# Performance work log

Measured on AMD Instinct MI355X. Metric: run time of the kernel, lower is better.

The kernel has to match this reference:

```python
import jax, jax.numpy as jnp
import numpy as np

N_NODES = 50000
N_EDGES = 640000
D = 128
BN_EPS = 1e-5


def setup_inputs() -> dict:
    key = jax.random.key(0)
    k1, k2, k3 = jax.random.split(key, 3)
    x = jax.random.normal(k1, (N_NODES, D), dtype=jnp.float32)
    # Glorot-ish weight for GCNConv linear
    W = jax.random.normal(k2, (D, D), dtype=jnp.float32) * (1.0 / np.sqrt(D))
    b = jnp.zeros((D,), dtype=jnp.float32)
    gamma = jnp.ones((D,), dtype=jnp.float32)
    beta = jnp.zeros((D,), dtype=jnp.float32)
    edge_index = jax.random.randint(k3, (2, N_EDGES), 0, N_NODES, dtype=jnp.int64)
    return {"x": x, "W": W, "b": b, "gamma": gamma, "beta": beta, "edge_index": edge_index}


def reference(x, W, b, gamma, beta, edge_index):
    N = x.shape[0]
    # --- GCNConv: x' = D^{-1/2} (A + I) D^{-1/2} (x W) + b ---
    xw = x @ W  # [N, D]
    loops = jnp.arange(N, dtype=edge_index.dtype)
    src = jnp.concatenate([edge_index[0], loops])  # [E+N]
    dst = jnp.concatenate([edge_index[1], loops])
    ones = jnp.ones(src.shape[0], dtype=x.dtype)
    deg = jax.ops.segment_sum(ones, dst, num_segments=N)  # in-degree incl. self-loop
    dinv = jnp.where(deg > 0, jax.lax.rsqrt(deg), 0.0)
    norm = dinv[src] * dinv[dst]  # [E+N]
    msg = xw[src] * norm[:, None]  # [E+N, D] gathered + scaled messages
    h = jax.ops.segment_sum(msg, dst, num_segments=N) + b  # scatter-add aggregation
    # --- BatchNorm1d (training-mode batch stats over nodes, biased var) ---
    mean = jnp.mean(h, axis=0)
    var = jnp.mean(jnp.square(h - mean), axis=0)
    h = (h - mean) * jax.lax.rsqrt(var + BN_EPS) * gamma + beta
    # --- activation (relu) ---
    h = jax.nn.relu(h)
    # --- residual (in_channels == out_channels) ---
    h = x + h
    # --- dropout: identity in eval mode for deterministic reference ---
    return h
```

## Files before the change

kernel.cpp:

```cpp
#include <hip/hip_runtime.h>

#define DCH 128
#define ROWS 16
#define BN_EPS 1e-5f

typedef unsigned short u16;
typedef __attribute__((ext_vector_type(8))) short short8;
typedef __attribute__((ext_vector_type(4))) float floatx4;

__device__ __forceinline__ float bf2f(u16 u) {
    return __uint_as_float(((unsigned)u) << 16);
}
__device__ __forceinline__ u16 f2bf(float f) {
    unsigned u = __float_as_uint(f);
    u += 0x7FFFu + ((u >> 16) & 1u);
    return (u16)(u >> 16);
}
__device__ __forceinline__ float ldf(const void* p, int i, int isbf) {
    return isbf ? bf2f(((const u16*)p)[i]) : ((const float*)p)[i];
}

__global__ void prep_kernel(const int* ei, int ewords, const u16* xw, int* ws_i,
                            const void* W, u16* Wb, float* zbase, int zn) {
    int t = threadIdx.x;
    if (blockIdx.x == 0) {
        __shared__ int s_nz, s_hits;
        if (t == 0) { s_nz = 0; s_hits = 0; }
        __syncthreads();
        int nz = 0;
        for (int i = t; i < 1024; i += 256) {
            int w = 2 * i + 1;
            if (w < ewords) nz |= ei[w];
        }
        if (nz) atomicOr(&s_nz, 1);
        unsigned m = (xw[2 * t] >> 8) & 0x7F;
        if (m >= 0x3B && m <= 0x43) atomicAdd(&s_hits, 1);
        __syncthreads();
        int isbf = (s_hits >= 128) ? 1 : 0;
        if (t == 0) {
            ws_i[0] = (s_nz == 0) ? 1 : 0;
            ws_i[1] = isbf;
            ws_i[2] = 0;
        }
        for (int idx = t; idx < DCH * DCH; idx += 256) {
            int j = idx & 7, lane = (idx >> 3) & 63, kk = (idx >> 9) & 3, nt = idx >> 11;
            int k = kk * 32 + (lane >> 4) * 8 + j;
            int n = nt * 16 + (lane & 15);
            Wb[idx] = f2bf(ldf(W, k * DCH + n, isbf));
        }
    } else {
        int stride = (gridDim.x - 1) * 256;
        for (int i = (blockIdx.x - 1) * 256 + t; i < zn; i += stride) zbase[i] = 0.f;
    }
}

__global__ void zero_kernel(float* p, int n) {
    int stride = gridDim.x * 256;
    for (int i = blockIdx.x * 256 + threadIdx.x; i < n; i += stride) p[i] = 0.f;
}

__global__ void paint_kernel(u16* out, int n, unsigned val) {
    int stride = gridDim.x * 256;
    for (int i = blockIdx.x * 256 + threadIdx.x; i < n; i += stride) out[i] = (u16)val;
}

__global__ void detect_kernel(const int* ei, int ewords, const u16* xw, int* ws_i) {
    __shared__ int s_nz, s_hits;
    int t = threadIdx.x;
    if (t == 0) { s_nz = 0; s_hits = 0; }
    __syncthreads();
    int nz = 0;
    for (int i = t; i < 1024; i += 256) {
        int w = 2 * i + 1;
        if (w < ewords) nz |= ei[w];
    }
    if (nz) atomicOr(&s_nz, 1);
    unsigned m = (xw[2 * t] >> 8) & 0x7F;
    if (m >= 0x3B && m <= 0x43) atomicAdd(&s_hits, 1);
    __syncthreads();
    if (t == 0) {
        ws_i[0] = (s_nz == 0) ? 1 : 0;
        ws_i[1] = (s_hits >= 128) ? 1 : 0;
        ws_i[2] = 0;
    }
}

__global__ void deg_kernel(const int* ei, int E, int* ws_i, int* deg, int N) {
    int is64 = ws_i[0];
    int i = blockIdx.x * 256 + threadIdx.x;
    int e0 = 2 * i;
    if (e0 >= E) return;
    int d0, d1 = -1, s0, s1 = 0;
    if (is64) {
        int4 sp = *(const int4*)&ei[2 * e0];
        int4 dp = *(const int4*)&ei[2 * E + 2 * e0];
        s0 = sp.x; s1 = sp.z; d0 = dp.x; d1 = dp.z;
    } else {
        int2 sp = *(const int2*)&ei[e0];
        int2 dp = *(const int2*)&ei[E + e0];
        s0 = sp.x; s1 = sp.y; d0 = dp.x; d1 = dp.y;
    }
    if (((unsigned)s0 >= (unsigned)N) || ((unsigned)d0 >= (unsigned)N))
        atomicOr(&ws_i[2], 2);
    atomicAdd(&deg[min(max(d0, 0), N - 1)], 1);
    if (e0 + 1 < E) {
        if (((unsigned)s1 >= (unsigned)N) || ((unsigned)d1 >= (unsigned)N))
            atomicOr(&ws_i[2], 2);
        atomicAdd(&deg[min(max(d1, 0), N - 1)], 1);
    }
}

__global__ void dinv_kernel(const int* deg, float* dinv, int N, int* ws_i) {
    int i = blockIdx.x * 256 + threadIdx.x;
    if (i < N) {
        float v = rsqrtf((float)(deg[i] + 1));
        if (!(v > 0.f && v <= 1.001f)) atomicOr(&ws_i[2], 4);
        dinv[i] = v;
    }
}

__global__ void scanA_kernel(const int* deg, int* part, int N) {
    int base = blockIdx.x * 1024 + threadIdx.x * 4;
    int s = 0;
    #pragma unroll
    for (int j = 0; j < 4; ++j) {
        int i = base + j;
        if (i < N) s += deg[i];
    }
    #pragma unroll
    for (int o = 1; o < 64; o <<= 1) s += __shfl_xor(s, o, 64);
    __shared__ int ws4[4];
    if ((threadIdx.x & 63) == 0) ws4[threadIdx.x >> 6] = s;
    __syncthreads();
    if (threadIdx.x == 0) part[blockIdx.x] = ws4[0] + ws4[1] + ws4[2] + ws4[3];
}

__global__ void scanB_kernel(int* part, int P) {
    __shared__ int wsum[4];
    int t = threadIdx.x, lane = t & 63, w = t >> 6;
    int v = (t < P) ? part[t] : 0;
    int sc = v;
    #pragma unroll
    for (int o = 1; o < 64; o <<= 1) {
        int u = __shfl_up(sc, o, 64);
        if (lane >= o) sc += u;
    }
    if (lane == 63) wsum[w] = sc;
    __syncthreads();
    if (t < 4) {
        int s = wsum[t];
        #pragma unroll
        for (int o = 1; o < 4; o <<= 1) {
            int u = __shfl_up(s, o, 4);
            if (t >= o) s += u;
        }
        wsum[t] = s;
    }
    __syncthreads();
    int excl = sc - v + (w ? wsum[w - 1] : 0);
    if (t < P) part[t] = excl;
}

__global__ void scanC_kernel(int* deg_cursor, const int* part, int* rowptr,
                             float* dinv, int N) {
    __shared__ int wsum[4];
    int t = threadIdx.x, lane = t & 63, w = t >> 6;
    int base = blockIdx.x * 1024 + t * 4;
    int v[4], ts = 0;
    #pragma unroll
    for (int j = 0; j < 4; ++j) {
        int i = base + j;
        v[j] = (i < N) ? deg_cursor[i] : 0;
        ts += v[j];
    }
    int sc = ts;
    #pragma unroll
    for (int o = 1; o < 64; o <<= 1) {
        int u = __shfl_up(sc, o, 64);
        if (lane >= o) sc += u;
    }
    if (lane == 63) wsum[w] = sc;
    __syncthreads();
    if (t < 4) {
        int s = wsum[t];
        #pragma unroll
        for (int o = 1; o < 4; o <<= 1) {
            int u = __shfl_up(s, o, 4);
            if (t >= o) s += u;
        }
        wsum[t] = s;
    }
    __syncthreads();
    int run = sc - ts + (w ? wsum[w - 1] : 0) + part[blockIdx.x];
    #pragma unroll
    for (int j = 0; j < 4; ++j) {
        int i = base + j;
        if (i < N) {
            deg_cursor[i] = run;
            run += v[j];
            rowptr[i + 1] = run;
            dinv[i] = rsqrtf((float)(v[j] + 1));
        }
    }
    if (blockIdx.x == 0 && t == 0) rowptr[0] = 0;
}

__global__ void fillcsr_kernel(const int* ei, int E, const int* ws_i,
                               int* cursor, int* col, int N) {
    int is64 = ws_i[0];
    int i = blockIdx.x * 256 + threadIdx.x;
    int e0 = 2 * i;
    if (e0 >= E) return;
    int d0, d1 = 0, s0, s1 = 0;
    if (is64) {
        int4 sp = *(const int4*)&ei[2 * e0];
        int4 dp = *(const int4*)&ei[2 * E + 2 * e0];
        s0 = sp.x; s1 = sp.z; d0 = dp.x; d1 = dp.z;
    } else {
        int2 sp = *(const int2*)&ei[e0];
        int2 dp = *(const int2*)&ei[E + e0];
        s0 = sp.x; s1 = sp.y; d0 = dp.x; d1 = dp.y;
    }
    s0 = min(max(s0, 0), N - 1);
    d0 = min(max(d0, 0), N - 1);
    int pos0 = atomicAdd(&cursor[d0], 1);
    col[pos0] = s0;
    if (e0 + 1 < E) {
        s1 = min(max(s1, 0), N - 1);
        d1 = min(max(d1, 0), N - 1);
        int pos1 = atomicAdd(&cursor[d1], 1);
        col[pos1] = s1;
    }
}

__global__ void gemm_mfma_kernel(const void* x, const u16* Wb, const float* dinv,
                                 const int* ws_i, u16* y, int N) {
    int isbf = ws_i[1];
    int t = threadIdx.x;
    int wv = t >> 6, lane = t & 63;
    int quad = lane >> 4, l16 = lane & 15;
    int r0 = blockIdx.x * 64 + wv * 16;
    int rl = min(r0 + l16, N - 1);
    short8 a[4];
    if (isbf) {
        const u16* xp = (const u16*)x + (size_t)rl * DCH + quad * 8;
        #pragma unroll
        for (int kk = 0; kk < 4; ++kk)
            a[kk] = *(const short8*)(xp + kk * 32);
    } else {
        const float* xp = (const float*)x + (size_t)rl * DCH + quad * 8;
        #pragma unroll
        for (int kk = 0; kk < 4; ++kk) {
            float4 f0 = *(const float4*)(xp + kk * 32);
            float4 f1 = *(const float4*)(xp + kk * 32 + 4);
            short8 aa;
            aa[0] = (short)f2bf(f0.x); aa[1] = (short)f2bf(f0.y);
            aa[2] = (short)f2bf(f0.z); aa[3] = (short)f2bf(f0.w);
            aa[4] = (short)f2bf(f1.x); aa[5] = (short)f2bf(f1.y);
            aa[6] = (short)f2bf(f1.z); aa[7] = (short)f2bf(f1.w);
            a[kk] = aa;
        }
    }
    floatx4 acc[8];
    #pragma unroll
    for (int i = 0; i < 8; ++i) acc[i] = (floatx4)(0.f);
    #pragma unroll
    for (int nt = 0; nt < 8; ++nt) {
        #pragma unroll
        for (int kk = 0; kk < 4; ++kk) {
            short8 bfr = *(const short8*)&Wb[(((nt << 2) | kk) * 64 + lane) * 8];
            acc[nt] = __builtin_amdgcn_mfma_f32_16x16x32_bf16(a[kk], bfr, acc[nt], 0, 0, 0);
        }
    }
    #pragma unroll
    for (int i = 0; i < 4; ++i) {
        int row = r0 + quad * 4 + i;
        if (row < N) {
            float dv = dinv[row];
            #pragma unroll
            for (int nt = 0; nt < 8; ++nt)
                y[(size_t)row * DCH + nt * 16 + l16] = f2bf(acc[nt][i] * dv);
        }
    }
}

__global__ __launch_bounds__(256, 8)
void gather_stats_kernel(const int* rowptr, const int* col, const u16* y,
                         const float* dinv, const void* b, const int* ws_i,
                         float* h, float* sums, float* sumsq, int N) {
    int isbf = ws_i[1];
    int t = threadIdx.x;
    int hw = t >> 5;
    int l32 = t & 31;
    int c0 = l32 * 4;
    float bb[4];
    #pragma unroll
    for (int k = 0; k < 4; ++k) bb[k] = ldf(b, c0 + k, isbf);
    float ps[4] = {0.f, 0.f, 0.f, 0.f}, pq[4] = {0.f, 0.f, 0.f, 0.f};
    int stream_id = blockIdx.x * 8 + hw;
    int nstreams = gridDim.x * 8;
    for (int n = stream_id; n < N; n += nstreams) {
        uint2 qs = *(const uint2*)&y[(size_t)n * DCH + c0];
        float a0[4] = { bf2f((u16)(qs.x & 0xFFFF)), bf2f((u16)(qs.x >> 16)),
                        bf2f((u16)(qs.y & 0xFFFF)), bf2f((u16)(qs.y >> 16)) };
        float a1[4] = {0.f, 0.f, 0.f, 0.f};
        float a2[4] = {0.f, 0.f, 0.f, 0.f};
        float a3[4] = {0.f, 0.f, 0.f, 0.f};
        int beg = rowptr[n], end = rowptr[n + 1];
        int j = beg;
        for (; j + 3 < end; j += 4) {
            int s0 = col[j], s1 = col[j + 1], s2 = col[j + 2], s3 = col[j + 3];
            uint2 q0 = *(const uint2*)&y[(size_t)s0 * DCH + c0];
            uint2 q1 = *(const uint2*)&y[(size_t)s1 * DCH + c0];
            uint2 q2 = *(const uint2*)&y[(size_t)s2 * DCH + c0];
            uint2 q3 = *(const uint2*)&y[(size_t)s3 * DCH + c0];
            a0[0] += bf2f((u16)(q0.x & 0xFFFF)); a0[1] += bf2f((u16)(q0.x >> 16));
            a0[2] += bf2f((u16)(q0.y & 0xFFFF)); a0[3] += bf2f((u16)(q0.y >> 16));
            a1[0] += bf2f((u16)(q1.x & 0xFFFF)); a1[1] += bf2f((u16)(q1.x >> 16));
            a1[2] += bf2f((u16)(q1.y & 0xFFFF)); a1[3] += bf2f((u16)(q1.y >> 16));
            a2[0] += bf2f((u16)(q2.x & 0xFFFF)); a2[1] += bf2f((u16)(q2.x >> 16));
            a2[2] += bf2f((u16)(q2.y & 0xFFFF)); a2[3] += bf2f((u16)(q2.y >> 16));
            a3[0] += bf2f((u16)(q3.x & 0xFFFF)); a3[1] += bf2f((u16)(q3.x >> 16));
            a3[2] += bf2f((u16)(q3.y & 0xFFFF)); a3[3] += bf2f((u16)(q3.y >> 16));
        }
        for (; j < end; ++j) {
            uint2 q0 = *(const uint2*)&y[(size_t)col[j] * DCH + c0];
            a0[0] += bf2f((u16)(q0.x & 0xFFFF)); a0[1] += bf2f((u16)(q0.x >> 16));
            a0[2] += bf2f((u16)(q0.y & 0xFFFF)); a0[3] += bf2f((u16)(q0.y >> 16));
        }
        float dn = dinv[n];
        float4 o;
        o.x = fmaf((a0[0] + a1[0]) + (a2[0] + a3[0]), dn, bb[0]);
        o.y = fmaf((a0[1] + a1[1]) + (a2[1] + a3[1]), dn, bb[1]);
        o.z = fmaf((a0[2] + a1[2]) + (a2[2] + a3[2]), dn, bb[2]);
        o.w = fmaf((a0[3] + a1[3]) + (a2[3] + a3[3]), dn, bb[3]);
        *(float4*)&h[(size_t)n * DCH + c0] = o;
        ps[0] += o.x; pq[0] += o.x * o.x;
        ps[1] += o.y; pq[1] += o.y * o.y;
        ps[2] += o.z; pq[2] += o.z * o.z;
        ps[3] += o.w; pq[3] += o.w * o.w;
    }
    __shared__ float lps[8][DCH], lpq[8][DCH];
    #pragma unroll
    for (int k = 0; k < 4; ++k) { lps[hw][c0 + k] = ps[k]; lpq[hw][c0 + k] = pq[k]; }
    __syncthreads();
    if (t < DCH) {
        int ch = (t + blockIdx.x * 16) & 127;
        float s = 0.f, q = 0.f;
        #pragma unroll
        for (int i = 0; i < 8; ++i) { s += lps[i][ch]; q += lpq[i][ch]; }
        atomicAdd(&sums[ch], s);
        atomicAdd(&sumsq[ch], q);
    }
}

__global__ void gemm_valu_kernel(const void* x, const void* W, const float* dinv,
                                 const int* ws_i, void* y, int N) {
    __shared__ float WsF[64 * DCH];
    __shared__ float xs[ROWS * DCH];
    int isbf = ws_i[1];
    int t = threadIdx.x;
    int r0 = blockIdx.x * ROWS;
    for (int i = t; i < ROWS * DCH; i += 256) {
        int r = r0 + (i >> 7);
        xs[i] = (r < N) ? ldf(x, r * DCH + (i & 127), isbf) : 0.f;
    }
    int d = t & 127, rh = t >> 7;
    float s[8];
    #pragma unroll
    for (int j = 0; j < 8; ++j) s[j] = 0.f;
    for (int half = 0; half < 2; ++half) {
        __syncthreads();
        for (int i = t; i < 64 * DCH; i += 256)
            WsF[i] = ldf(W, half * 64 * DCH + i, isbf);
        __syncthreads();
        #pragma unroll
        for (int j = 0; j < 8; ++j) {
            int rr = rh + 2 * j;
            float a = s[j];
            #pragma unroll 16
            for (int k = 0; k < 64; ++k)
                a = fmaf(xs[rr * DCH + half * 64 + k], WsF[k * DCH + d], a);
            s[j] = a;
        }
    }
    #pragma unroll
    for (int j = 0; j < 8; ++j) {
        int r = r0 + rh + 2 * j;
        if (r < N) {
            float v = s[j] * dinv[r];
            if (isbf) ((u16*)y)[r * DCH + d] = f2bf(v);
            else      ((float*)y)[r * DCH + d] = v;
        }
    }
}

__global__ void scatter_kernel(const int* ei, int E, const int* ws_i,
                               const void* y, float* acc, int N) {
    int is64 = ws_i[0], isbf = ws_i[1];
    int gid = blockIdx.x * 256 + threadIdx.x;
    int e = gid >> 5;
    if (e >= E) return;
    int c0 = (gid & 31) * 4;
    int s = is64 ? ei[2 * e] : ei[e];
    int d = is64 ? ei[2 * E + 2 * e] : ei[E + e];
    s = min(max(s, 0), N - 1);
    d = min(max(d, 0), N - 1);
    float v0, v1, v2, v3;
    if (isbf) {
        uint2 raw = *(const uint2*)&((const u16*)y)[s * DCH + c0];
        v0 = bf2f((u16)(raw.x & 0xFFFF)); v1 = bf2f((u16)(raw.x >> 16));
        v2 = bf2f((u16)(raw.y & 0xFFFF)); v3 = bf2f((u16)(raw.y >> 16));
    } else {
        float4 raw = *(const float4*)&((const float*)y)[s * DCH + c0];
        v0 = raw.x; v1 = raw.y; v2 = raw.z; v3 = raw.w;
    }
    float* a = &acc[d * DCH + c0];
    atomicAdd(a + 0, v0);
    atomicAdd(a + 1, v1);
    atomicAdd(a + 2, v2);
    atomicAdd(a + 3, v3);
}

__global__ void bnstat_kernel(const void* y, float* acc, const float* dinv,
                              const void* b, int* ws_i,
                              float* sums, float* sumsq, int total) {
    int isbf = ws_i[1];
    int t = threadIdx.x;
    int d = t & 127;
    float bb = ldf(b, d, isbf);
    float ps = 0.f, pq = 0.f;
    int stride = gridDim.x * 256;
    for (int i = blockIdx.x * 256 + t; i < total; i += stride) {
        int r = i >> 7;
        float yv = isbf ? bf2f(((const u16*)y)[i]) : ((const float*)y)[i];
        float v = (yv + acc[i]) * dinv[r] + bb;
        acc[i] = v;
        ps += v;
        pq += v * v;
    }
    __shared__ float ls[256], lq[256];
    ls[t] = ps; lq[t] = pq;
    __syncthreads();
    if (t < 128) {
        atomicAdd(&sums[d], ls[t] + ls[t + 128]);
        atomicAdd(&sumsq[d], lq[t] + lq[t + 128]);
    }
}

__global__ void out_kernel(const float* h, const void* x,
                           const void* gamma, const void* beta,
                           int* ws_i, const float* sums, const float* sumsq,
                           void* out, int total, float invN) {
    __shared__ float sc[DCH], sh[DCH];
    int isbf = ws_i[1];
    int t = threadIdx.x;
    if (t < DCH) {
        float mean = sums[t] * invN;
        float var = fmaxf(sumsq[t] * invN - mean * mean, 0.f);
        float s = ldf(gamma, t, isbf) * rsqrtf(var + BN_EPS);
        if (!(var < 1e8f && fabsf(s) < 1e6f)) atomicOr(&ws_i[2], 32);
        sc[t] = s;
        sh[t] = ldf(beta, t, isbf) - mean * s;
    }
    __syncthreads();
    int total4 = total >> 2;
    int stride = gridDim.x * 256;
    for (int i4 = blockIdx.x * 256 + t; i4 < total4; i4 += stride) {
        int i = i4 * 4;
        int d = i & 127;
        float4 hv = *(const float4*)&h[i];
        float v0 = fmaf(hv.x, sc[d], sh[d]);
        float v1 = fmaf(hv.y, sc[d + 1], sh[d + 1]);
        float v2 = fmaf(hv.z, sc[d + 2], sh[d + 2]);
        float v3 = fmaf(hv.w, sc[d + 3], sh[d + 3]);
        if (isbf) {
            uint2 xv = *(const uint2*)&((const u16*)x)[i];
            v0 = fmaxf(v0, 0.f) + bf2f((u16)(xv.x & 0xFFFF));
            v1 = fmaxf(v1, 0.f) + bf2f((u16)(xv.x >> 16));
            v2 = fmaxf(v2, 0.f) + bf2f((u16)(xv.y & 0xFFFF));
            v3 = fmaxf(v3, 0.f) + bf2f((u16)(xv.y >> 16));
            uint2 ov;
            ov.x = (unsigned)f2bf(v0) | ((unsigned)f2bf(v1) << 16);
            ov.y = (unsigned)f2bf(v2) | ((unsigned)f2bf(v3) << 16);
            *(uint2*)&((u16*)out)[i] = ov;
        } else {
            float4 xv = *(const float4*)&((const float*)x)[i];
            float4 ov;
            ov.x = fmaxf(v0, 0.f) + xv.x;
            ov.y = fmaxf(v1, 0.f) + xv.y;
            ov.z = fmaxf(v2, 0.f) + xv.z;
            ov.w = fmaxf(v3, 0.f) + xv.w;
            *(float4*)&((float*)out)[i] = ov;
        }
    }
}

__global__ void diag_kernel(const int* ws_i, void* out, int n) {
    int e = ws_i[2];
    if (!e) return;
    int isbf = ws_i[1];
    float v = 4096.f + 32.f * (float)(e & 63);
    int stride = gridDim.x * 256;
    if (isbf) {
        u16 code = f2bf(v);
        for (int i = blockIdx.x * 256 + threadIdx.x; i < n; i += stride)
            ((u16*)out)[i] = code;
    } else {
        for (int i = blockIdx.x * 256 + threadIdx.x; i < n; i += stride)
            ((float*)out)[i] = v;
    }
}

extern "C" void kernel_launch(void* const* d_in, const int* in_sizes, int n_in,
                              void* d_out, int out_size, void* d_ws, size_t ws_size,
                              hipStream_t stream) {
    const void* x     = d_in[0];
    const void* W     = d_in[1];
    const void* b     = d_in[2];
    const void* gamma = d_in[3];
    const void* beta  = d_in[4];
    const int*  ei    = (const int*)d_in[5];

    const int N  = in_sizes[0] / DCH;
    const int E  = in_sizes[5] / 2;
    const int ND = N * DCH;
    const int P  = (N + 1023) / 1024;

    char* wsb = (char*)d_ws;
    int*  ws_i = (int*)wsb;

    size_t o_wb   = 64;
    size_t o_deg  = o_wb + 32768;
    size_t o_sum  = o_deg + 4 * (size_t)N;
    size_t o_sq   = o_sum + 512;
    size_t o_rp   = o_sq + 512;
    size_t o_dinv = o_rp + 4 * ((size_t)N + 1) + 4;
    size_t o_part = o_dinv + 4 * (size_t)N;
    size_t o_h    = (o_part + 1024 + 255) & ~(size_t)255;
    size_t o_col  = o_h + 4 * (size_t)ND;
    size_t need_csr = o_col + 4 * (size_t)E;

    (void)hipGetLastError();

    if (ws_size >= need_csr) {
        u16*   Wb    = (u16*)(wsb + o_wb);
        int*   deg   = (int*)(wsb + o_deg);
        float* sums  = (float*)(wsb + o_sum);
        float* sumsq = (float*)(wsb + o_sq);
        int*   rowptr= (int*)(wsb + o_rp);
        float* dinv  = (float*)(wsb + o_dinv);
        int*   part  = (int*)(wsb + o_part);
        float* h     = (float*)(wsb + o_h);
        int*   col   = (int*)(wsb + o_col);
        u16*   y     = (u16*)d_out;

        prep_kernel<<<65, 256, 0, stream>>>(ei, 2 * E, (const u16*)x, ws_i,
                                            W, Wb, (float*)(wsb + o_deg), N + 256);
        deg_kernel<<<(E / 2 + 255) / 256, 256, 0, stream>>>(ei, E, ws_i, deg, N);
        scanA_kernel<<<P, 256, 0, stream>>>(deg, part, N);
        scanB_kernel<<<1, 256, 0, stream>>>(part, P);
        scanC_kernel<<<P, 256, 0, stream>>>(deg, part, rowptr, dinv, N);
        fillcsr_kernel<<<(E / 2 + 255) / 256, 256, 0, stream>>>(ei, E, ws_i, deg, col, N);
        gemm_mfma_kernel<<<(N + 63) / 64, 256, 0, stream>>>(x, Wb, dinv, ws_i, y, N);
        gather_stats_kernel<<<2560, 256, 0, stream>>>(rowptr, col, y, dinv, b, ws_i,
                                                      h, sums, sumsq, N);
        out_kernel<<<1024, 256, 0, stream>>>(h, x, gamma, beta, ws_i, sums, sumsq,
                                             d_out, ND, 1.0f / (float)N);
        diag_kernel<<<512, 256, 0, stream>>>(ws_i, d_out, out_size);
    } else {
        int*   deg   = (int*)(wsb + 16);
        float* dinv  = (float*)(wsb + 16 + 4 * (size_t)N);
        float* sums  = (float*)(wsb + 16 + 8 * (size_t)N);
        float* sumsq = sums + DCH;
        float* acc   = sumsq + DCH;
        size_t need = 16 + 8 * (size_t)N + 1024 + 4 * (size_t)ND;
        if (ws_size < need) {
            int mb = (int)(ws_size >> 20); if (mb > 127) mb = 127;
            float v = 2048.f + 16.f * (float)mb;
            unsigned u; __builtin_memcpy(&u, &v, 4);
            paint_kernel<<<1024, 256, 0, stream>>>((u16*)d_out, out_size, u >> 16);
            return;
        }
        detect_kernel<<<1, 256, 0, stream>>>(ei, 2 * E, (const u16*)x, ws_i);
        zero_kernel<<<2048, 256, 0, stream>>>((float*)(wsb + 16), 2 * N + 256 + ND);
        deg_kernel<<<(E / 2 + 255) / 256, 256, 0, stream>>>(ei, E, ws_i, deg, N);
        dinv_kernel<<<(N + 255) / 256, 256, 0, stream>>>(deg, dinv, N, ws_i);
        gemm_valu_kernel<<<(N + ROWS - 1) / ROWS, 256, 0, stream>>>(x, W, dinv, ws_i, d_out, N);
        scatter_kernel<<<(E * 32 + 255) / 256, 256, 0, stream>>>(ei, E, ws_i, d_out, acc, N);
        bnstat_kernel<<<240, 256, 0, stream>>>(d_out, acc, dinv, b, ws_i, sums, sumsq, ND);
        out_kernel<<<256, 256, 0, stream>>>(acc, x, gamma, beta, ws_i, sums, sumsq,
                                            d_out, ND, 1.0f / (float)N);
        diag_kernel<<<512, 256, 0, stream>>>(ws_i, d_out, out_size);
    }

    if (hipGetLastError() != hipSuccess)
        hipMemsetAsync(d_out, 0x42, (size_t)out_size * 2, stream);
}
```

Before: 277.1 us.

## Split fused gather/BN-stats kernel into separate gather and stats kernels

```diff
diff --git a/kernel.cpp b/kernel.cpp
--- a/kernel.cpp
+++ b/kernel.cpp
@@ -284,73 +284,67 @@
     }
 }
 
-__global__ __launch_bounds__(256, 8)
-void gather_stats_kernel(const int* rowptr, const int* col, const u16* y,
-                         const float* dinv, const void* b, const int* ws_i,
-                         float* h, float* sums, float* sumsq, int N) {
+__global__ void gather_kernel(const int* rowptr, const int* col, const u16* y,
+                              const float* dinv, const void* b, const int* ws_i,
+                              float* h, int N) {
     int isbf = ws_i[1];
     int t = threadIdx.x;
     int hw = t >> 5;
     int l32 = t & 31;
     int c0 = l32 * 4;
-    float bb[4];
-    #pragma unroll
-    for (int k = 0; k < 4; ++k) bb[k] = ldf(b, c0 + k, isbf);
-    float ps[4] = {0.f, 0.f, 0.f, 0.f}, pq[4] = {0.f, 0.f, 0.f, 0.f};
-    int stream_id = blockIdx.x * 8 + hw;
-    int nstreams = gridDim.x * 8;
-    for (int n = stream_id; n < N; n += nstreams) {
-        uint2 qs = *(const uint2*)&y[(size_t)n * DCH + c0];
-        float a0[4] = { bf2f((u16)(qs.x & 0xFFFF)), bf2f((u16)(qs.x >> 16)),
-                        bf2f((u16)(qs.y & 0xFFFF)), bf2f((u16)(qs.y >> 16)) };
-        float a1[4] = {0.f, 0.f, 0.f, 0.f};
-        float a2[4] = {0.f, 0.f, 0.f, 0.f};
-        float a3[4] = {0.f, 0.f, 0.f, 0.f};
-        int beg = rowptr[n], end = rowptr[n + 1];
-        int j = beg;
-        for (; j + 3 < end; j += 4) {
-            int s0 = col[j], s1 = col[j + 1], s2 = col[j + 2], s3 = col[j + 3];
-            uint2 q0 = *(const uint2*)&y[(size_t)s0 * DCH + c0];
-            uint2 q1 = *(const uint2*)&y[(size_t)s1 * DCH + c0];
-            uint2 q2 = *(const uint2*)&y[(size_t)s2 * DCH + c0];
-            uint2 q3 = *(const uint2*)&y[(size_t)s3 * DCH + c0];
-            a0[0] += bf2f((u16)(q0.x & 0xFFFF)); a0[1] += bf2f((u16)(q0.x >> 16));
-            a0[2] += bf2f((u16)(q0.y & 0xFFFF)); a0[3] += bf2f((u16)(q0.y >> 16));
-            a1[0] += bf2f((u16)(q1.x & 0xFFFF)); a1[1] += bf2f((u16)(q1.x >> 16));
-            a1[2] += bf2f((u16)(q1.y & 0xFFFF)); a1[3] += bf2f((u16)(q1.y >> 16));
-            a2[0] += bf2f((u16)(q2.x & 0xFFFF)); a2[1] += bf2f((u16)(q2.x >> 16));
-            a2[2] += bf2f((u16)(q2.y & 0xFFFF)); a2[3] += bf2f((u16)(q2.y >> 16));
-            a3[0] += bf2f((u16)(q3.x & 0xFFFF)); a3[1] += bf2f((u16)(q3.x >> 16));
-            a3[2] += bf2f((u16)(q3.y & 0xFFFF)); a3[3] += bf2f((u16)(q3.y >> 16));
-        }
-        for (; j < end; ++j) {
-            uint2 q0 = *(const uint2*)&y[(size_t)col[j] * DCH + c0];
-            a0[0] += bf2f((u16)(q0.x & 0xFFFF)); a0[1] += bf2f((u16)(q0.x >> 16));
-            a0[2] += bf2f((u16)(q0.y & 0xFFFF)); a0[3] += bf2f((u16)(q0.y >> 16));
-        }
-        float dn = dinv[n];
-        float4 o;
-        o.x = fmaf((a0[0] + a1[0]) + (a2[0] + a3[0]), dn, bb[0]);
-        o.y = fmaf((a0[1] + a1[1]) + (a2[1] + a3[1]), dn, bb[1]);
-        o.z = fmaf((a0[2] + a1[2]) + (a2[2] + a3[2]), dn, bb[2]);
-        o.w = fmaf((a0[3] + a1[3]) + (a2[3] + a3[3]), dn, bb[3]);
-        *(float4*)&h[(size_t)n * DCH + c0] = o;
-        ps[0] += o.x; pq[0] += o.x * o.x;
-        ps[1] += o.y; pq[1] += o.y * o.y;
-        ps[2] += o.z; pq[2] += o.z * o.z;
-        ps[3] += o.w; pq[3] += o.w * o.w;
-    }
-    __shared__ float lps[8][DCH], lpq[8][DCH];
-    #pragma unroll
-    for (int k = 0; k < 4; ++k) { lps[hw][c0 + k] = ps[k]; lpq[hw][c0 + k] = pq[k]; }
-    __syncthreads();
-    if (t < DCH) {
-        int ch = (t + blockIdx.x * 16) & 127;
-        float s = 0.f, q = 0.f;
-        #pragma unroll
-        for (int i = 0; i < 8; ++i) { s += lps[i][ch]; q += lpq[i][ch]; }
-        atomicAdd(&sums[ch], s);
-        atomicAdd(&sumsq[ch], q);
+    int n = blockIdx.x * 8 + hw;
+    if (n >= N) return;
+    uint2 qs = *(const uint2*)&y[(size_t)n * DCH + c0];
+    float a0[4] = { bf2f((u16)(qs.x & 0xFFFF)), bf2f((u16)(qs.x >> 16)),
+                    bf2f((u16)(qs.y & 0xFFFF)), bf2f((u16)(qs.y >> 16)) };
+    float a1[4] = {0.f, 0.f, 0.f, 0.f};
+    float a2[4] = {0.f, 0.f, 0.f, 0.f};
+    float a3[4] = {0.f, 0.f, 0.f, 0.f};
+    int beg = rowptr[n], end = rowptr[n + 1];
+    int j = beg;
+    for (; j + 3 < end; j += 4) {
+        int s0 = col[j], s1 = col[j + 1], s2 = col[j + 2], s3 = col[j + 3];
+        uint2 q0 = *(const uint2*)&y[(size_t)s0 * DCH + c0];
+        uint2 q1 = *(const uint2*)&y[(size_t)s1 * DCH + c0];
+        uint2 q2 = *(const uint2*)&y[(size_t)s2 * DCH + c0];
+        uint2 q3 = *(const uint2*)&y[(size_t)s3 * DCH + c0];
+        a0[0] += bf2f((u16)(q0.x & 0xFFFF)); a0[1] += bf2f((u16)(q0.x >> 16));
+        a0[2] += bf2f((u16)(q0.y & 0xFFFF)); a0[3] += bf2f((u16)(q0.y >> 16));
+        a1[0] += bf2f((u16)(q1.x & 0xFFFF)); a1[1] += bf2f((u16)(q1.x >> 16));
+        a1[2] += bf2f((u16)(q1.y & 0xFFFF)); a1[3] += bf2f((u16)(q1.y >> 16));
+        a2[0] += bf2f((u16)(q2.x & 0xFFFF)); a2[1] += bf2f((u16)(q2.x >> 16));
+        a2[2] += bf2f((u16)(q2.y & 0xFFFF)); a2[3] += bf2f((u16)(q2.y >> 16));
+        a3[0] += bf2f((u16)(q3.x & 0xFFFF)); a3[1] += bf2f((u16)(q3.x >> 16));
+        a3[2] += bf2f((u16)(q3.y & 0xFFFF)); a3[3] += bf2f((u16)(q3.y >> 16));
+    }
+    for (; j < end; ++j) {
+        uint2 q0 = *(const uint2*)&y[(size_t)col[j] * DCH + c0];
+        a0[0] += bf2f((u16)(q0.x & 0xFFFF)); a0[1] += bf2f((u16)(q0.x >> 16));
+        a0[2] += bf2f((u16)(q0.y & 0xFFFF)); a0[3] += bf2f((u16)(q0.y >> 16));
+    }
+    float dn = dinv[n];
+    float4 o;
+    o.x = fmaf((a0[0] + a1[0]) + (a2[0] + a3[0]), dn, ldf(b, c0, isbf));
+    o.y = fmaf((a0[1] + a1[1]) + (a2[1] + a3[1]), dn, ldf(b, c0 + 1, isbf));
+    o.z = fmaf((a0[2] + a1[2]) + (a2[2] + a3[2]), dn, ldf(b, c0 + 2, isbf));
+    o.w = fmaf((a0[3] + a1[3]) + (a2[3] + a3[3]), dn, ldf(b, c0 + 3, isbf));
+    *(float4*)&h[(size_t)n * DCH + c0] = o;
+}
+
+__global__ void bnstat2_kernel(const float* h, float* sums, float* sumsq, int total) {
+    int t = threadIdx.x, d = t & 127;
+    float ps = 0.f, pq = 0.f;
+    int stride = gridDim.x * 256;
+    for (int i = blockIdx.x * 256 + t; i < total; i += stride) {
+        float v = h[i];
+        ps += v; pq += v * v;
+    }
+    __shared__ float ls[256], lq[256];
+    ls[t] = ps; lq[t] = pq;
+    __syncthreads();
+    if (t < 128) {
+        atomicAdd(&sums[d], ls[t] + ls[t + 128]);
+        atomicAdd(&sumsq[d], lq[t] + lq[t + 128]);
     }
 }
 
@@ -563,8 +557,8 @@
         scanC_kernel<<<P, 256, 0, stream>>>(deg, part, rowptr, dinv, N);
         fillcsr_kernel<<<(E / 2 + 255) / 256, 256, 0, stream>>>(ei, E, ws_i, deg, col, N);
         gemm_mfma_kernel<<<(N + 63) / 64, 256, 0, stream>>>(x, Wb, dinv, ws_i, y, N);
-        gather_stats_kernel<<<2560, 256, 0, stream>>>(rowptr, col, y, dinv, b, ws_i,
-                                                      h, sums, sumsq, N);
+        gather_kernel<<<(N + 7) / 8, 256, 0, stream>>>(rowptr, col, y, dinv, b, ws_i, h, N);
+        bnstat2_kernel<<<512, 256, 0, stream>>>(h, sums, sumsq, ND);
         out_kernel<<<1024, 256, 0, stream>>>(h, x, gamma, beta, ws_i, sums, sumsq,
                                              d_out, ND, 1.0f / (float)N);
         diag_kernel<<<512, 256, 0, stream>>>(ws_i, d_out, out_size);
```

New measurement: 255.3 us. 1.09x faster.
